# Optimization experiments

Measured on AMD Instinct MI355X. Metric: run time of the kernel, lower is better.

## Reference

```python
import jax, jax.numpy as jnp
import numpy as np


def setup_inputs() -> dict:
    key = jax.random.key(0)
    k1, k2, k3, k4 = jax.random.split(key, 4)
    B, S, K, N = 2, 1024, 4096, 4096
    x = jax.random.normal(k1, (B, S, K), dtype=jnp.float32)
    # int8 weights in [-128, 127]
    weight = jax.random.randint(k2, (N, K), -128, 128, dtype=jnp.int8)
    # per-output-channel dequant scales (small positive values)
    scales = jax.random.uniform(k3, (N,), dtype=jnp.float32, minval=0.005, maxval=0.02)
    bias = jax.random.normal(k4, (N,), dtype=jnp.float32) * 0.1
    return {"x": x, "weight": weight, "scales": scales, "bias": bias}


def reference(x, weight, scales, bias):
    # F.linear(x, weight.to(x.dtype)): [B,S,K] @ [N,K]^T -> [B,S,N]
    w = weight.astype(x.dtype)
    y = jnp.einsum('bsk,nk->bsn', x, w)
    # per-output-channel scale + bias epilogue
    return y * scales + bias
```

## Files before the change

kernel.cpp:

```cpp
#include <hip/hip_runtime.h>
#include <hip/hip_bf16.h>
#include <stdint.h>

#define M_DIM 2048
#define N_DIM 4096
#define K_DIM 4096

#define BM 256
#define BN 128
#define BK 128

#define ATILE (BM * BK)
#define BTILE (BN * BK)

typedef __attribute__((ext_vector_type(4))) int int4v;

__device__ __forceinline__ void load_lds16(const void* g, void* l) {
    __builtin_amdgcn_global_load_lds(
        (const __attribute__((address_space(1))) void*)g,
        (__attribute__((address_space(3))) void*)l,
        16, 0, 0);
}

__global__ __launch_bounds__(256) void quant_x(const float* __restrict__ x,
                                               int8_t* __restrict__ Aq,
                                               float* __restrict__ sx) {
    const int row = blockIdx.x;
    const int tid = threadIdx.x;
    const float4* xr = (const float4*)(x + (size_t)row * K_DIM);

    float4 v[4];
    float mx = 0.f;
#pragma unroll
    for (int p = 0; p < 4; p++) {
        v[p] = xr[p * 256 + tid];
        mx = fmaxf(mx, fmaxf(fmaxf(fabsf(v[p].x), fabsf(v[p].y)),
                             fmaxf(fabsf(v[p].z), fabsf(v[p].w))));
    }
#pragma unroll
    for (int off = 32; off >= 1; off >>= 1)
        mx = fmaxf(mx, __shfl_xor(mx, off, 64));

    __shared__ float wmax[4];
    __shared__ float smax;
    if ((tid & 63) == 0) wmax[tid >> 6] = mx;
    __syncthreads();
    if (tid == 0) {
        float m = fmaxf(fmaxf(wmax[0], wmax[1]), fmaxf(wmax[2], wmax[3]));
        m = fmaxf(m, 1e-20f);
        smax = m;
        sx[row] = m * (1.0f / 127.0f);
    }
    __syncthreads();
    const float inv = 127.0f / smax;

    int* out = (int*)Aq + (size_t)row * (K_DIM / 4);
#pragma unroll
    for (int p = 0; p < 4; p++) {
        int q0 = (int)__builtin_rintf(v[p].x * inv);
        int q1 = (int)__builtin_rintf(v[p].y * inv);
        int q2 = (int)__builtin_rintf(v[p].z * inv);
        int q3 = (int)__builtin_rintf(v[p].w * inv);
        q0 = max(-127, min(127, q0)); q1 = max(-127, min(127, q1));
        q2 = max(-127, min(127, q2)); q3 = max(-127, min(127, q3));
        out[p * 256 + tid] = (q0 & 255) | ((q1 & 255) << 8) |
                             ((q2 & 255) << 16) | ((q3 & 255) << 24);
    }
}

__global__ __launch_bounds__(256) void cvt_w8(const int* __restrict__ w,
                                              int8_t* __restrict__ Bq) {
    size_t i = ((size_t)blockIdx.x * 256 + threadIdx.x) * 16;
    int4 a0 = *(const int4*)(w + i);
    int4 a1 = *(const int4*)(w + i + 4);
    int4 a2 = *(const int4*)(w + i + 8);
    int4 a3 = *(const int4*)(w + i + 12);
    uint4 t;
    t.x = (a0.x & 255) | ((a0.y & 255) << 8) | ((a0.z & 255) << 16) | ((a0.w & 255) << 24);
    t.y = (a1.x & 255) | ((a1.y & 255) << 8) | ((a1.z & 255) << 16) | ((a1.w & 255) << 24);
    t.z = (a2.x & 255) | ((a2.y & 255) << 8) | ((a2.z & 255) << 16) | ((a2.w & 255) << 24);
    t.w = (a3.x & 255) | ((a3.y & 255) << 8) | ((a3.z & 255) << 16) | ((a3.w & 255) << 24);
    *(uint4*)(Bq + i) = t;
}


__global__ __launch_bounds__(1024, 4) void gemm_bt_i8(
    const int8_t* __restrict__ A,
    const int8_t* __restrict__ B,
    const float*  __restrict__ sx,
    const float*  __restrict__ scales,
    const float*  __restrict__ bias,
    float* __restrict__ C)
{
    __shared__ __align__(16) int8_t As[2 * ATILE];
    __shared__ __align__(16) int8_t Bs[2 * BTILE];

    const int tid  = threadIdx.x;
    const int bm   = blockIdx.y;
    const int bn   = blockIdx.x;
    const int lane = tid & 63;
    const int wave = tid >> 6;
    const int wm   = (wave >> 2) * 64;
    const int wn   = (wave & 3) * 32;
    const int l16  = lane & 15;
    const int quad = lane >> 4;
    const int swz  = l16 & 7;

    const int srow = tid >> 3;
    const int cgp  = tid & 7;
    const int cgl  = cgp ^ (srow & 7);

    const int8_t* ga0 = A + (size_t)(bm * BM + srow)       * K_DIM + cgl * 16;
    const int8_t* ga1 = A + (size_t)(bm * BM + 128 + srow) * K_DIM + cgl * 16;
    const int8_t* gb0 = B + (size_t)(bn * BN + srow)       * K_DIM + cgl * 16;
    const int la0 = srow * BK + cgp * 16;
    const int la1 = ATILE / 2 + la0;

    load_lds16(ga0, As + la0);
    load_lds16(ga1, As + la1);
    load_lds16(gb0, Bs + la0);

    int4v acc[4][2] = {};

    int cur = 0;
    for (int k0 = 0; k0 < K_DIM; k0 += BK, cur ^= 1) {
        __syncthreads();

        const int kn = k0 + BK;
        if (kn < K_DIM) {
            const int nb = (cur ^ 1);
            load_lds16(ga0 + kn, As + nb * ATILE + la0);
            load_lds16(ga1 + kn, As + nb * ATILE + la1);
            load_lds16(gb0 + kn, Bs + nb * BTILE + la0);
        }

        const int8_t* Ab = As + cur * ATILE;
        const int8_t* Bb = Bs + cur * BTILE;

#pragma unroll
        for (int h = 0; h < 2; h++) {
            const int cp = (h * 4 + quad) ^ swz;
            int4v af[4], bfr[2];
#pragma unroll
            for (int i = 0; i < 4; i++)
                af[i] = *(const int4v*)(Ab + (wm + i * 16 + l16) * BK + cp * 16);
#pragma unroll
            for (int j = 0; j < 2; j++)
                bfr[j] = *(const int4v*)(Bb + (wn + j * 16 + l16) * BK + cp * 16);
#pragma unroll
            for (int i = 0; i < 4; i++)
#pragma unroll
                for (int j = 0; j < 2; j++)
                    acc[i][j] = __builtin_amdgcn_mfma_i32_16x16x64_i8(
                        af[i], bfr[j], acc[i][j], 0, 0, 0);
        }
    }

    float sxr[16];
#pragma unroll
    for (int i = 0; i < 4; i++)
#pragma unroll
        for (int r = 0; r < 4; r++)
            sxr[i * 4 + r] = sx[bm * BM + wm + i * 16 + quad * 4 + r];

#pragma unroll
    for (int j = 0; j < 2; j++) {
        const int col = bn * BN + wn + j * 16 + l16;
        const float s = scales[col];
        const float b = bias[col];
#pragma unroll
        for (int i = 0; i < 4; i++) {
            const int row0 = bm * BM + wm + i * 16 + quad * 4;
#pragma unroll
            for (int r = 0; r < 4; r++) {
                C[(size_t)(row0 + r) * N_DIM + col] =
                    (float)acc[i][j][r] * (sxr[i * 4 + r] * s) + b;
            }
        }
    }
}


extern "C" void kernel_launch(void* const* d_in, const int* in_sizes, int n_in,
                              void* d_out, int out_size, void* d_ws, size_t ws_size,
                              hipStream_t stream) {
    const float* x      = (const float*)d_in[0];
    const int*   w      = (const int*)d_in[1];
    const float* scales = (const float*)d_in[2];
    const float* bias   = (const float*)d_in[3];
    float*       out    = (float*)d_out;

    int8_t* Aq = (int8_t*)d_ws;
    int8_t* Bq = (int8_t*)d_ws + (size_t)M_DIM * K_DIM;
    float*  sx = (float*)((int8_t*)d_ws + (size_t)(M_DIM + N_DIM) * K_DIM);

    quant_x<<<M_DIM, 256, 0, stream>>>(x, Aq, sx);
    cvt_w8<<<(int)((size_t)N_DIM * K_DIM / 16 / 256), 256, 0, stream>>>(w, Bq);

    dim3 grid(N_DIM / BN, M_DIM / BM);
    gemm_bt_i8<<<grid, 1024, 0, stream>>>(Aq, Bq, sx, scales, bias, out);
}
```

Measured before the change: 168.7 us.

## Use 128x128 tiles, 256-thread blocks, register-staged prefetch instead of direct LDS loads

Shrinks the GEMM block tile from 256x128 with 16 waves to 128x128 with 4 waves, each wave covering a 64x64 sub-tile (16 accumulators). Global-to-LDS direct loads are replaced by loads into registers that are issued two K-steps ahead and written to the alternate LDS buffer. The barrier moves to the end of each iteration. The aim is more MFMA work per LDS fragment read and better overlap of global latency, at the cost of more registers per thread and fewer waves per CU.

```diff
diff --git a/kernel.cpp b/kernel.cpp
--- a/kernel.cpp
+++ b/kernel.cpp
@@ -6,7 +6,7 @@
 #define N_DIM 4096
 #define K_DIM 4096
 
-#define BM 256
+#define BM 128
 #define BN 128
 #define BK 128
 
@@ -14,13 +14,6 @@
 #define BTILE (BN * BK)
 
 typedef __attribute__((ext_vector_type(4))) int int4v;
-
-__device__ __forceinline__ void load_lds16(const void* g, void* l) {
-    __builtin_amdgcn_global_load_lds(
-        (const __attribute__((address_space(1))) void*)g,
-        (__attribute__((address_space(3))) void*)l,
-        16, 0, 0);
-}
 
 __global__ __launch_bounds__(256) void quant_x(const float* __restrict__ x,
                                                int8_t* __restrict__ Aq,
@@ -84,7 +77,7 @@
 }
 
 
-__global__ __launch_bounds__(1024, 4) void gemm_bt_i8(
+__global__ __launch_bounds__(256, 2) void gemm_bt_i8(
     const int8_t* __restrict__ A,
     const int8_t* __restrict__ B,
     const float*  __restrict__ sx,
@@ -100,8 +93,8 @@
     const int bn   = blockIdx.x;
     const int lane = tid & 63;
     const int wave = tid >> 6;
-    const int wm   = (wave >> 2) * 64;
-    const int wn   = (wave & 3) * 32;
+    const int wm   = (wave >> 1) * 64;
+    const int wn   = (wave & 1) * 64;
     const int l16  = lane & 15;
     const int quad = lane >> 4;
     const int swz  = l16 & 7;
@@ -110,50 +103,72 @@
     const int cgp  = tid & 7;
     const int cgl  = cgp ^ (srow & 7);
 
-    const int8_t* ga0 = A + (size_t)(bm * BM + srow)       * K_DIM + cgl * 16;
-    const int8_t* ga1 = A + (size_t)(bm * BM + 128 + srow) * K_DIM + cgl * 16;
-    const int8_t* gb0 = B + (size_t)(bn * BN + srow)       * K_DIM + cgl * 16;
-    const int la0 = srow * BK + cgp * 16;
-    const int la1 = ATILE / 2 + la0;
-
-    load_lds16(ga0, As + la0);
-    load_lds16(ga1, As + la1);
-    load_lds16(gb0, Bs + la0);
-
-    int4v acc[4][2] = {};
+    const int8_t* gA = A + (size_t)(bm * BM + srow) * K_DIM + cgl * 16;
+    const int8_t* gB = B + (size_t)(bn * BN + srow) * K_DIM + cgl * 16;
+    const int lw = tid * 16;
+
+    uint4 ra[4], rb[4];
+
+#pragma unroll
+    for (int p = 0; p < 4; p++) {
+        ra[p] = *(const uint4*)(gA + (size_t)p * 32 * K_DIM);
+        rb[p] = *(const uint4*)(gB + (size_t)p * 32 * K_DIM);
+    }
+#pragma unroll
+    for (int p = 0; p < 4; p++) {
+        *(uint4*)(As + p * 4096 + lw) = ra[p];
+        *(uint4*)(Bs + p * 4096 + lw) = rb[p];
+    }
+#pragma unroll
+    for (int p = 0; p < 4; p++) {
+        ra[p] = *(const uint4*)(gA + BK + (size_t)p * 32 * K_DIM);
+        rb[p] = *(const uint4*)(gB + BK + (size_t)p * 32 * K_DIM);
+    }
+    __syncthreads();
+
+    int4v acc[4][4] = {};
 
     int cur = 0;
     for (int k0 = 0; k0 < K_DIM; k0 += BK, cur ^= 1) {
-        __syncthreads();
-
         const int kn = k0 + BK;
         if (kn < K_DIM) {
-            const int nb = (cur ^ 1);
-            load_lds16(ga0 + kn, As + nb * ATILE + la0);
-            load_lds16(ga1 + kn, As + nb * ATILE + la1);
-            load_lds16(gb0 + kn, Bs + nb * BTILE + la0);
+            const int nb = cur ^ 1;
+#pragma unroll
+            for (int p = 0; p < 4; p++) {
+                *(uint4*)(As + nb * ATILE + p * 4096 + lw) = ra[p];
+                *(uint4*)(Bs + nb * BTILE + p * 4096 + lw) = rb[p];
+            }
+            if (kn + BK < K_DIM) {
+#pragma unroll
+                for (int p = 0; p < 4; p++) {
+                    ra[p] = *(const uint4*)(gA + kn + BK + (size_t)p * 32 * K_DIM);
+                    rb[p] = *(const uint4*)(gB + kn + BK + (size_t)p * 32 * K_DIM);
+                }
+            }
         }
 
         const int8_t* Ab = As + cur * ATILE;
         const int8_t* Bb = Bs + cur * BTILE;
 
 #pragma unroll
-        for (int h = 0; h < 2; h++) {
-            const int cp = (h * 4 + quad) ^ swz;
-            int4v af[4], bfr[2];
+        for (int s = 0; s < 2; s++) {
+            const int cp = (s * 4 + quad) ^ swz;
+            int4v af[4], bfr[4];
 #pragma unroll
             for (int i = 0; i < 4; i++)
                 af[i] = *(const int4v*)(Ab + (wm + i * 16 + l16) * BK + cp * 16);
 #pragma unroll
-            for (int j = 0; j < 2; j++)
+            for (int j = 0; j < 4; j++)
                 bfr[j] = *(const int4v*)(Bb + (wn + j * 16 + l16) * BK + cp * 16);
 #pragma unroll
             for (int i = 0; i < 4; i++)
 #pragma unroll
-                for (int j = 0; j < 2; j++)
+                for (int j = 0; j < 4; j++)
                     acc[i][j] = __builtin_amdgcn_mfma_i32_16x16x64_i8(
                         af[i], bfr[j], acc[i][j], 0, 0, 0);
         }
+
+        __syncthreads();
     }
 
     float sxr[16];
@@ -164,7 +179,7 @@
             sxr[i * 4 + r] = sx[bm * BM + wm + i * 16 + quad * 4 + r];
 
 #pragma unroll
-    for (int j = 0; j < 2; j++) {
+    for (int j = 0; j < 4; j++) {
         const int col = bn * BN + wn + j * 16 + l16;
         const float s = scales[col];
         const float b = bias[col];
@@ -198,5 +213,5 @@
     cvt_w8<<<(int)((size_t)N_DIM * K_DIM / 16 / 256), 256, 0, stream>>>(w, Bq);
 
     dim3 grid(N_DIM / BN, M_DIM / BM);
-    gemm_bt_i8<<<grid, 1024, 0, stream>>>(Aq, Bq, sx, scales, bias, out);
-}
+    gemm_bt_i8<<<grid, 256, 0, stream>>>(Aq, Bq, sx, scales, bias, out);
+}
```

Measured after the change: 237.7 us. +40.9%, slower.
